# Kernel optimization log

Measured on AMD Instinct MI355X. Metric: run time of the kernel, lower is better.

## Reference

```python
import jax, jax.numpy as jnp
import numpy as np

B, N, D, H = 8, 384, 256, 1024

def setup_inputs() -> dict:
    key = jax.random.key(0)
    ks = jax.random.split(key, 8)
    x = jax.random.normal(ks[0], (B, N, D), jnp.float32)
    adj = jnp.ones((B, N, N), jnp.float32)
    box_num = jax.random.randint(ks[1], (B, 1), 1, N + 1).astype(jnp.int64)
    box_num = box_num.at[0, 0].set(N)  # original code assumes max(box_num) == N
    fc1_w = jax.random.normal(ks[2], (H, D), jnp.float32) * (1.0 / np.sqrt(D))
    fc1_b = jnp.zeros((H,), jnp.float32)
    fc2_w = jax.random.normal(ks[3], (D, H), jnp.float32) * (1.0 / np.sqrt(H))
    fc2_b = jnp.zeros((D,), jnp.float32)
    learn_w = jax.random.uniform(ks[4], (D,), jnp.float32)  # uniform_(0,1) init
    return {"x": x, "adj": adj, "box_num": box_num,
            "fc1_w": fc1_w, "fc1_b": fc1_b, "fc2_w": fc2_w, "fc2_b": fc2_b,
            "learn_w": learn_w}

def reference(x, adj, box_num, fc1_w, fc1_b, fc2_w, fc2_b, learn_w):
    # mlp: fc2(relu(fc1(x)))  -> x_hat (B,N,D)
    x_hat = jnp.maximum(x @ fc1_w.T + fc1_b, 0.0) @ fc2_w.T + fc2_b
    # dynamic mask: -1 where either node i or j is padding, 0 otherwise
    valid = jnp.arange(N)[None, :] < box_num            # (B,N)
    pair_valid = valid[:, None, :] & valid[:, :, None]  # (B,N,N)
    mask = jnp.where(pair_valid, 0.0, -1.0)             # (B,N,N)
    # pairwise weighted L1 distance: einsum('bijd,d->bij', |x_i - x_j| + mask, w)
    # mask broadcasts over d, so its contribution is mask * sum(w) (same math,
    # avoids a second (B,N,N,D) materialization)
    absdiff = jnp.abs(x_hat[:, :, None, :] - x_hat[:, None, :, :])  # (B,N,N,D)
    dist = jnp.einsum('bijd,d->bij', absdiff, learn_w) + mask * jnp.sum(learn_w)
    out = jax.nn.leaky_relu(dist, negative_slope=0.01)
    out = out - jnp.max(out, axis=-1, keepdims=True)
    soft_adj = adj * jnp.exp(out)
    soft_adj = soft_adj / jnp.sum(soft_adj, axis=-1, keepdims=True) + 1e-10
    return soft_adj, x_hat
```

## Files before the change

kernel.cpp:

```cpp
#include <hip/hip_runtime.h>
#include <math.h>

#define B_ 8
#define N_ 384
#define D_ 256
#define H_ 1024

typedef __bf16 bh;
typedef __bf16 bf16x8 __attribute__((ext_vector_type(8)));
typedef float  f32x4  __attribute__((ext_vector_type(4)));
typedef _Float16 h2 __attribute__((ext_vector_type(2)));

#define LDK 40

#if __has_builtin(__builtin_amdgcn_fdot2)
#define FDOT2(a,b,c) __builtin_amdgcn_fdot2((a),(b),(c),false)
#else
#define FDOT2(a,b,c) ((c) + (float)(a).x*(float)(b).x + (float)(a).y*(float)(b).y)
#endif

__device__ inline h2 habs2(h2 x) {
    unsigned u = __builtin_bit_cast(unsigned, x) & 0x7fff7fffu;
    return __builtin_bit_cast(h2, u);
}

__device__ inline void split2(float v, bh& h, bh& l) {
    h = (bh)v;
    l = (bh)(v - (float)h);
}

__device__ inline int load_boxnum(const int* __restrict__ p, int b) {
    bool is64 = ((p[1] | p[3] | p[5] | p[7]) == 0);
    return is64 ? p[2 * b] : p[b];
}

__global__ __launch_bounds__(256) void gemm1_kernel(
        const float* __restrict__ A,
        const float* __restrict__ W,
        const float* __restrict__ bias,
        bh* __restrict__ Ch, bh* __restrict__ Cl)
{
    __shared__ __align__(16) bh AhS[64 * LDK], AlS[64 * LDK], WhS[64 * LDK], WlS[64 * LDK];
    const int tid = threadIdx.x;
    const int m0 = blockIdx.y * 64, n0 = blockIdx.x * 64;
    const int r = tid >> 2, kq = (tid & 3) * 8;
    const int lane = tid & 63, wv_ = tid >> 6;
    const int wm = (wv_ & 1) * 32, wn = (wv_ >> 1) * 32;
    const int l15 = lane & 15, q = lane >> 4;

    f32x4 acc[2][2] = {};
    for (int k0 = 0; k0 < 256; k0 += 32) {
        const float* ap = A + (size_t)(m0 + r) * 256 + k0 + kq;
        const float* wp = W + (size_t)(n0 + r) * 256 + k0 + kq;
        float4 a0 = *(const float4*)ap;
        float4 a1 = *(const float4*)(ap + 4);
        float4 w0 = *(const float4*)wp;
        float4 w1 = *(const float4*)(wp + 4);
        float av[8] = {a0.x, a0.y, a0.z, a0.w, a1.x, a1.y, a1.z, a1.w};
        float wf[8] = {w0.x, w0.y, w0.z, w0.w, w1.x, w1.y, w1.z, w1.w};
        bf16x8 ah, al, wh, wl;
        #pragma unroll
        for (int i = 0; i < 8; i++) {
            bh h, l;
            split2(av[i], h, l); ah[i] = h; al[i] = l;
            split2(wf[i], h, l); wh[i] = h; wl[i] = l;
        }
        __syncthreads();
        *(bf16x8*)&AhS[r * LDK + kq] = ah;  *(bf16x8*)&AlS[r * LDK + kq] = al;
        *(bf16x8*)&WhS[r * LDK + kq] = wh;  *(bf16x8*)&WlS[r * LDK + kq] = wl;
        __syncthreads();
        bf16x8 fah[2], fal[2], fwh[2], fwl[2];
        #pragma unroll
        for (int mi = 0; mi < 2; mi++) {
            int row = wm + mi * 16 + l15;
            fah[mi] = *(const bf16x8*)&AhS[row * LDK + q * 8];
            fal[mi] = *(const bf16x8*)&AlS[row * LDK + q * 8];
        }
        #pragma unroll
        for (int ni = 0; ni < 2; ni++) {
            int row = wn + ni * 16 + l15;
            fwh[ni] = *(const bf16x8*)&WhS[row * LDK + q * 8];
            fwl[ni] = *(const bf16x8*)&WlS[row * LDK + q * 8];
        }
        #pragma unroll
        for (int mi = 0; mi < 2; mi++)
            #pragma unroll
            for (int ni = 0; ni < 2; ni++) {
                acc[mi][ni] = __builtin_amdgcn_mfma_f32_16x16x32_bf16(fah[mi], fwh[ni], acc[mi][ni], 0, 0, 0);
                acc[mi][ni] = __builtin_amdgcn_mfma_f32_16x16x32_bf16(fah[mi], fwl[ni], acc[mi][ni], 0, 0, 0);
                acc[mi][ni] = __builtin_amdgcn_mfma_f32_16x16x32_bf16(fal[mi], fwh[ni], acc[mi][ni], 0, 0, 0);
            }
    }
    #pragma unroll
    for (int ni = 0; ni < 2; ni++) {
        int col = n0 + wn + ni * 16 + l15;
        float bb = bias[col];
        #pragma unroll
        for (int mi = 0; mi < 2; mi++)
            #pragma unroll
            for (int reg = 0; reg < 4; reg++) {
                int row = m0 + wm + mi * 16 + q * 4 + reg;
                float v = fmaxf(acc[mi][ni][reg] + bb, 0.f);
                bh h, l; split2(v, h, l);
                size_t off = (size_t)row * H_ + col;
                Ch[off] = h; Cl[off] = l;
            }
    }
}

__global__ __launch_bounds__(128) void gemm2_kernel(
        const bh* __restrict__ Ah_, const bh* __restrict__ Al_,
        const float* __restrict__ W,
        const float* __restrict__ bias,
        float* __restrict__ C)
{
    __shared__ __align__(16) bh AhS[64 * LDK], AlS[64 * LDK], WhS[32 * LDK], WlS[32 * LDK];
    const int tid = threadIdx.x;
    const int m0 = blockIdx.y * 64, n0 = blockIdx.x * 32;
    const int lane = tid & 63, wv_ = tid >> 6;
    const int wm = wv_ * 32;
    const int l15 = lane & 15, q = lane >> 4;
    const int ra = tid >> 1, ka = (tid & 1) * 16;
    const int rw = tid >> 2, kw = (tid & 3) * 8;

    f32x4 acc[2][2] = {};
    for (int k0 = 0; k0 < 1024; k0 += 32) {
        const bh* ahp = Ah_ + (size_t)(m0 + ra) * H_ + k0 + ka;
        const bh* alp = Al_ + (size_t)(m0 + ra) * H_ + k0 + ka;
        bf16x8 h0 = *(const bf16x8*)ahp, h1 = *(const bf16x8*)(ahp + 8);
        bf16x8 l0 = *(const bf16x8*)alp, l1 = *(const bf16x8*)(alp + 8);
        const float* wp = W + (size_t)(n0 + rw) * H_ + k0 + kw;
        float4 w0 = *(const float4*)wp, w1 = *(const float4*)(wp + 4);
        float wf[8] = {w0.x, w0.y, w0.z, w0.w, w1.x, w1.y, w1.z, w1.w};
        bf16x8 wh, wl;
        #pragma unroll
        for (int i = 0; i < 8; i++) { bh h, l; split2(wf[i], h, l); wh[i] = h; wl[i] = l; }
        __syncthreads();
        *(bf16x8*)&AhS[ra * LDK + ka] = h0;  *(bf16x8*)&AhS[ra * LDK + ka + 8] = h1;
        *(bf16x8*)&AlS[ra * LDK + ka] = l0;  *(bf16x8*)&AlS[ra * LDK + ka + 8] = l1;
        *(bf16x8*)&WhS[rw * LDK + kw] = wh;  *(bf16x8*)&WlS[rw * LDK + kw] = wl;
        __syncthreads();
        bf16x8 fah[2], fal[2], fwh[2], fwl[2];
        #pragma unroll
        for (int mi = 0; mi < 2; mi++) {
            int row = wm + mi * 16 + l15;
            fah[mi] = *(const bf16x8*)&AhS[row * LDK + q * 8];
            fal[mi] = *(const bf16x8*)&AlS[row * LDK + q * 8];
        }
        #pragma unroll
        for (int ni = 0; ni < 2; ni++) {
            int row = ni * 16 + l15;
            fwh[ni] = *(const bf16x8*)&WhS[row * LDK + q * 8];
            fwl[ni] = *(const bf16x8*)&WlS[row * LDK + q * 8];
        }
        #pragma unroll
        for (int mi = 0; mi < 2; mi++)
            #pragma unroll
            for (int ni = 0; ni < 2; ni++) {
                acc[mi][ni] = __builtin_amdgcn_mfma_f32_16x16x32_bf16(fah[mi], fwh[ni], acc[mi][ni], 0, 0, 0);
                acc[mi][ni] = __builtin_amdgcn_mfma_f32_16x16x32_bf16(fah[mi], fwl[ni], acc[mi][ni], 0, 0, 0);
                acc[mi][ni] = __builtin_amdgcn_mfma_f32_16x16x32_bf16(fal[mi], fwh[ni], acc[mi][ni], 0, 0, 0);
            }
    }
    #pragma unroll
    for (int ni = 0; ni < 2; ni++) {
        int col = n0 + ni * 16 + l15;
        float bb = bias[col];
        #pragma unroll
        for (int mi = 0; mi < 2; mi++)
            #pragma unroll
            for (int reg = 0; reg < 4; reg++) {
                int row = m0 + wm + mi * 16 + q * 4 + reg;
                C[(size_t)row * D_ + col] = acc[mi][ni][reg] + bb;
            }
    }
}

#define DLP 68
__global__ __launch_bounds__(256) void dist_kernel(const float* __restrict__ xhat,
                                                   const float* __restrict__ w,
                                                   const int* __restrict__ box_num,
                                                   float* __restrict__ dist) {
    __shared__ __align__(16) unsigned XiU[16 * DLP];
    __shared__ __align__(16) unsigned XjU[16 * DLP];
    const int bidx = blockIdx.x;
    const int b = bidx / 21;
    int p = bidx % 21;
    int ti = 0;
    while (p >= 6 - ti) { p -= 6 - ti; ti++; }
    const int tj = ti + p;
    const int i0 = ti * 64, j0 = tj * 64;

    const int tid = threadIdx.x;
    const int tx = tid & 15, ty = tid >> 4;
    const int lane = tid & 63;
    const int r = tid >> 2, kq = (tid & 3) * 8;
    const int kq2 = (tid & 3) * 4;

    float sumw = w[lane] + w[lane + 64] + w[lane + 128] + w[lane + 192];
    #pragma unroll
    for (int off = 32; off > 0; off >>= 1) sumw += __shfl_xor(sumw, off);

    const float* xb = xhat + (size_t)b * N_ * D_;
    float acc[4][4] = {};

    for (int k0 = 0; k0 < D_; k0 += 32) {
        h2 wk2[16];
        #pragma unroll
        for (int c = 0; c < 16; c++) {
            float2 wp = *(const float2*)&w[k0 + 2 * c];
            wk2[c] = (h2){(_Float16)wp.x, (_Float16)wp.y};
        }
        const float* ip = xb + (size_t)(i0 + r) * D_ + k0 + kq;
        const float* jp = xb + (size_t)(j0 + r) * D_ + k0 + kq;
        float4 i0v = *(const float4*)ip, i1v = *(const float4*)(ip + 4);
        float4 j0v = *(const float4*)jp, j1v = *(const float4*)(jp + 4);
        float fi[8] = {i0v.x, i0v.y, i0v.z, i0v.w, i1v.x, i1v.y, i1v.z, i1v.w};
        float fj[8] = {j0v.x, j0v.y, j0v.z, j0v.w, j1v.x, j1v.y, j1v.z, j1v.w};
        __syncthreads();
        #pragma unroll
        for (int c = 0; c < 4; c++) {
            h2 hi = (h2){(_Float16)fi[2 * c], (_Float16)fi[2 * c + 1]};
            h2 hj = (h2){(_Float16)fj[2 * c], (_Float16)fj[2 * c + 1]};
            XiU[(kq2 + c) * DLP + r] = __builtin_bit_cast(unsigned, hi);
            XjU[(kq2 + c) * DLP + r] = __builtin_bit_cast(unsigned, hj);
        }
        __syncthreads();
        #pragma unroll
        for (int k2 = 0; k2 < 16; k2++) {
            uint4 ar = *(const uint4*)&XiU[k2 * DLP + ty * 4];
            uint4 br = *(const uint4*)&XjU[k2 * DLP + tx * 4];
            h2 ai[4] = {__builtin_bit_cast(h2, ar.x), __builtin_bit_cast(h2, ar.y),
                        __builtin_bit_cast(h2, ar.z), __builtin_bit_cast(h2, ar.w)};
            h2 bj[4] = {__builtin_bit_cast(h2, br.x), __builtin_bit_cast(h2, br.y),
                        __builtin_bit_cast(h2, br.z), __builtin_bit_cast(h2, br.w)};
            h2 wv = wk2[k2];
            #pragma unroll
            for (int ii = 0; ii < 4; ii++)
                #pragma unroll
                for (int jj = 0; jj < 4; jj++) {
                    h2 d = habs2(ai[ii] - bj[jj]);
                    acc[ii][jj] = FDOT2(d, wv, acc[ii][jj]);
                }
        }
    }

    const int bn = load_boxnum(box_num, b);
    float m[4][4];
    #pragma unroll
    for (int ii = 0; ii < 4; ii++) {
        int i = i0 + ty * 4 + ii;
        bool vi = i < bn;
        #pragma unroll
        for (int jj = 0; jj < 4; jj++) {
            int j = j0 + tx * 4 + jj;
            float v = acc[ii][jj];
            if (!(vi && (j < bn))) v -= sumw;
            m[ii][jj] = v > 0.f ? v : 0.01f * v;
        }
    }
    #pragma unroll
    for (int ii = 0; ii < 4; ii++) {
        int i = i0 + ty * 4 + ii;
        float4 o = {m[ii][0], m[ii][1], m[ii][2], m[ii][3]};
        *(float4*)&dist[((size_t)b * N_ + i) * N_ + j0 + tx * 4] = o;
    }
    #pragma unroll
    for (int jj = 0; jj < 4; jj++) {
        int j = j0 + tx * 4 + jj;
        float4 o = {m[0][jj], m[1][jj], m[2][jj], m[3][jj]};
        *(float4*)&dist[((size_t)b * N_ + j) * N_ + i0 + ty * 4] = o;
    }
}

__global__ __launch_bounds__(256) void softmax_kernel(float* __restrict__ sa,
                                                      const float* __restrict__ adj) {
    const int row = blockIdx.x * 4 + (threadIdx.x >> 6);
    const int t = threadIdx.x & 63;
    float* prow = sa + (size_t)row * N_;
    const float* arow = adj + (size_t)row * N_;
    float v[6];
    float m = -1e30f;
    #pragma unroll
    for (int qq = 0; qq < 6; qq++) { v[qq] = prow[t + qq * 64]; m = fmaxf(m, v[qq]); }
    #pragma unroll
    for (int off = 32; off > 0; off >>= 1) m = fmaxf(m, __shfl_xor(m, off));
    float e[6];
    float s = 0.f;
    #pragma unroll
    for (int qq = 0; qq < 6; qq++) { e[qq] = arow[t + qq * 64] * expf(v[qq] - m); s += e[qq]; }
    #pragma unroll
    for (int off = 32; off > 0; off >>= 1) s += __shfl_xor(s, off);
    float inv = 1.0f / s;
    #pragma unroll
    for (int qq = 0; qq < 6; qq++) prow[t + qq * 64] = e[qq] * inv + 1e-10f;
}

extern "C" void kernel_launch(void* const* d_in, const int* in_sizes, int n_in,
                              void* d_out, int out_size, void* d_ws, size_t ws_size,
                              hipStream_t stream) {
    const float* x       = (const float*)d_in[0];
    const float* adj     = (const float*)d_in[1];
    const int*   box_num = (const int*)d_in[2];
    const float* fc1_w   = (const float*)d_in[3];
    const float* fc1_b   = (const float*)d_in[4];
    const float* fc2_w   = (const float*)d_in[5];
    const float* fc2_b   = (const float*)d_in[6];
    const float* learn_w = (const float*)d_in[7];

    float* soft_adj = (float*)d_out;
    float* xhat     = (float*)d_out + (size_t)B_ * N_ * N_;

    const int BN = B_ * N_;
    const size_t bytes_per_row = (size_t)H_ * 2 * 2;
    long long mr = (long long)(ws_size / bytes_per_row) & ~63LL;
    int max_rows = (int)((mr > BN) ? BN : mr);
    if (max_rows < 64) max_rows = 64;
    bh* c1h = (bh*)d_ws;
    bh* c1l = c1h + (size_t)max_rows * H_;

    for (int m0 = 0; m0 < BN; m0 += max_rows) {
        int rows = BN - m0; if (rows > max_rows) rows = max_rows;
        dim3 g1(H_ / 64, rows / 64);
        gemm1_kernel<<<g1, 256, 0, stream>>>(x + (size_t)m0 * D_, fc1_w, fc1_b, c1h, c1l);
        dim3 g2(D_ / 32, rows / 64);
        gemm2_kernel<<<g2, 128, 0, stream>>>(c1h, c1l, fc2_w, fc2_b, xhat + (size_t)m0 * D_);
    }

    dist_kernel<<<B_ * 21, 256, 0, stream>>>(xhat, learn_w, box_num, soft_adj);

    softmax_kernel<<<BN / 4, 256, 0, stream>>>(soft_adj, adj);
}
```

Before: 140.7 us.

## Pre-split GEMM operands to bf16 and use larger swizzled tiles with direct LDS loads

Adds a prep kernel that splits x, fc1_w and fc2_w into bf16 hi/lo pairs once, so the GEMMs no longer redo the split inside every tile. Both GEMMs are rewritten to use global_load_lds direct-to-LDS copies, XOR-swizzled LDS layouts, and larger tiles (128x128 for gemm1, 64x128 with K step 64 for gemm2) to raise reuse per block. The workspace chunking loop is removed, so the code now assumes the workspace holds all intermediates. It also adds an extra launch, and with fewer, larger blocks fewer CUs may be occupied.

```diff
diff --git a/kernel.cpp b/kernel.cpp
--- a/kernel.cpp
+++ b/kernel.cpp
@@ -7,11 +7,10 @@
 #define H_ 1024
 
 typedef __bf16 bh;
+typedef __bf16 bh4   __attribute__((ext_vector_type(4)));
 typedef __bf16 bf16x8 __attribute__((ext_vector_type(8)));
 typedef float  f32x4  __attribute__((ext_vector_type(4)));
 typedef _Float16 h2 __attribute__((ext_vector_type(2)));
-
-#define LDK 40
 
 #if __has_builtin(__builtin_amdgcn_fdot2)
 #define FDOT2(a,b,c) __builtin_amdgcn_fdot2((a),(b),(c),false)
@@ -19,6 +18,10 @@
 #define FDOT2(a,b,c) ((c) + (float)(a).x*(float)(b).x + (float)(a).y*(float)(b).y)
 #endif
 
+#define GLDS16(gp, lp) __builtin_amdgcn_global_load_lds( \
+    (const __attribute__((address_space(1))) unsigned*)(gp), \
+    (__attribute__((address_space(3))) unsigned*)(lp), 16, 0, 0)
+
 __device__ inline h2 habs2(h2 x) {
     unsigned u = __builtin_bit_cast(unsigned, x) & 0x7fff7fffu;
     return __builtin_bit_cast(h2, u);
@@ -34,143 +37,151 @@
     return is64 ? p[2 * b] : p[b];
 }
 
+__global__ __launch_bounds__(256) void prep_split(
+        const float* __restrict__ x, const float* __restrict__ w1, const float* __restrict__ w2,
+        bh* __restrict__ xh, bh* __restrict__ xl,
+        bh* __restrict__ w1h, bh* __restrict__ w1l,
+        bh* __restrict__ w2h, bh* __restrict__ w2l) {
+    const int blk = blockIdx.x;
+    const float* src; bh *dh, *dl; int idx;
+    if (blk < 768)       { src = x;  dh = xh;  dl = xl;  idx = blk * 256 + threadIdx.x; }
+    else if (blk < 1024) { src = w1; dh = w1h; dl = w1l; idx = (blk - 768) * 256 + threadIdx.x; }
+    else                 { src = w2; dh = w2h; dl = w2l; idx = (blk - 1024) * 256 + threadIdx.x; }
+    float4 v = ((const float4*)src)[idx];
+    float f[4] = {v.x, v.y, v.z, v.w};
+    bh4 hv, lv;
+    #pragma unroll
+    for (int i = 0; i < 4; i++) { bh h, l; split2(f[i], h, l); hv[i] = h; lv[i] = l; }
+    *(bh4*)&dh[4 * (size_t)idx] = hv;
+    *(bh4*)&dl[4 * (size_t)idx] = lv;
+}
+
 __global__ __launch_bounds__(256) void gemm1_kernel(
-        const float* __restrict__ A,
-        const float* __restrict__ W,
+        const bh* __restrict__ xh, const bh* __restrict__ xl,
+        const bh* __restrict__ w1h, const bh* __restrict__ w1l,
         const float* __restrict__ bias,
-        bh* __restrict__ Ch, bh* __restrict__ Cl)
-{
-    __shared__ __align__(16) bh AhS[64 * LDK], AlS[64 * LDK], WhS[64 * LDK], WlS[64 * LDK];
-    const int tid = threadIdx.x;
-    const int m0 = blockIdx.y * 64, n0 = blockIdx.x * 64;
-    const int r = tid >> 2, kq = (tid & 3) * 8;
-    const int lane = tid & 63, wv_ = tid >> 6;
-    const int wm = (wv_ & 1) * 32, wn = (wv_ >> 1) * 32;
+        bh* __restrict__ c1h, bh* __restrict__ c1l) {
+    __shared__ __align__(16) bh lds[16384];
+    const int tid = threadIdx.x, lane = tid & 63, w = tid >> 6;
+    const int m0 = blockIdx.y * 128, n0 = blockIdx.x * 128;
+    const int lr = lane >> 2, kb = lane & 3;
+    const int kbp = kb ^ ((lr >> 1) & 3);
+    const bh* psrc; int rowbase;
+    if (w == 0)      { psrc = xh;  rowbase = m0; }
+    else if (w == 1) { psrc = xl;  rowbase = m0; }
+    else if (w == 2) { psrc = w1h; rowbase = n0; }
+    else             { psrc = w1l; rowbase = n0; }
+    const bh* gsrc = psrc + (size_t)(rowbase + lr) * 256 + kbp * 8;
+    bh* lwb = &lds[w * 4096 + lane * 8];
     const int l15 = lane & 15, q = lane >> 4;
-
-    f32x4 acc[2][2] = {};
+    const int swq = q ^ ((l15 >> 1) & 3);
+    const int wm = (w & 1) * 64, wn = (w >> 1) * 64;
+
+    f32x4 acc[4][4] = {};
     for (int k0 = 0; k0 < 256; k0 += 32) {
-        const float* ap = A + (size_t)(m0 + r) * 256 + k0 + kq;
-        const float* wp = W + (size_t)(n0 + r) * 256 + k0 + kq;
-        float4 a0 = *(const float4*)ap;
-        float4 a1 = *(const float4*)(ap + 4);
-        float4 w0 = *(const float4*)wp;
-        float4 w1 = *(const float4*)(wp + 4);
-        float av[8] = {a0.x, a0.y, a0.z, a0.w, a1.x, a1.y, a1.z, a1.w};
-        float wf[8] = {w0.x, w0.y, w0.z, w0.w, w1.x, w1.y, w1.z, w1.w};
-        bf16x8 ah, al, wh, wl;
-        #pragma unroll
-        for (int i = 0; i < 8; i++) {
-            bh h, l;
-            split2(av[i], h, l); ah[i] = h; al[i] = l;
-            split2(wf[i], h, l); wh[i] = h; wl[i] = l;
-        }
-        __syncthreads();
-        *(bf16x8*)&AhS[r * LDK + kq] = ah;  *(bf16x8*)&AlS[r * LDK + kq] = al;
-        *(bf16x8*)&WhS[r * LDK + kq] = wh;  *(bf16x8*)&WlS[r * LDK + kq] = wl;
-        __syncthreads();
-        bf16x8 fah[2], fal[2], fwh[2], fwl[2];
-        #pragma unroll
-        for (int mi = 0; mi < 2; mi++) {
-            int row = wm + mi * 16 + l15;
-            fah[mi] = *(const bf16x8*)&AhS[row * LDK + q * 8];
-            fal[mi] = *(const bf16x8*)&AlS[row * LDK + q * 8];
-        }
-        #pragma unroll
-        for (int ni = 0; ni < 2; ni++) {
-            int row = wn + ni * 16 + l15;
-            fwh[ni] = *(const bf16x8*)&WhS[row * LDK + q * 8];
-            fwl[ni] = *(const bf16x8*)&WlS[row * LDK + q * 8];
-        }
-        #pragma unroll
-        for (int mi = 0; mi < 2; mi++)
-            #pragma unroll
-            for (int ni = 0; ni < 2; ni++) {
-                acc[mi][ni] = __builtin_amdgcn_mfma_f32_16x16x32_bf16(fah[mi], fwh[ni], acc[mi][ni], 0, 0, 0);
-                acc[mi][ni] = __builtin_amdgcn_mfma_f32_16x16x32_bf16(fah[mi], fwl[ni], acc[mi][ni], 0, 0, 0);
-                acc[mi][ni] = __builtin_amdgcn_mfma_f32_16x16x32_bf16(fal[mi], fwh[ni], acc[mi][ni], 0, 0, 0);
-            }
-    }
-    #pragma unroll
-    for (int ni = 0; ni < 2; ni++) {
+        __syncthreads();
+        #pragma unroll
+        for (int s = 0; s < 8; s++)
+            GLDS16(gsrc + (size_t)s * 4096 + k0, lwb + s * 512);
+        __syncthreads();
+        bf16x8 fa[4][2], fb[4][2];
+        #pragma unroll
+        for (int i = 0; i < 4; i++) {
+            int ra = wm + i * 16 + l15;
+            int rb = wn + i * 16 + l15;
+            fa[i][0] = *(const bf16x8*)&lds[        ra * 32 + swq * 8];
+            fa[i][1] = *(const bf16x8*)&lds[ 4096 + ra * 32 + swq * 8];
+            fb[i][0] = *(const bf16x8*)&lds[ 8192 + rb * 32 + swq * 8];
+            fb[i][1] = *(const bf16x8*)&lds[12288 + rb * 32 + swq * 8];
+        }
+        #pragma unroll
+        for (int mi = 0; mi < 4; mi++)
+            #pragma unroll
+            for (int ni = 0; ni < 4; ni++) {
+                acc[mi][ni] = __builtin_amdgcn_mfma_f32_16x16x32_bf16(fa[mi][0], fb[ni][0], acc[mi][ni], 0, 0, 0);
+                acc[mi][ni] = __builtin_amdgcn_mfma_f32_16x16x32_bf16(fa[mi][0], fb[ni][1], acc[mi][ni], 0, 0, 0);
+                acc[mi][ni] = __builtin_amdgcn_mfma_f32_16x16x32_bf16(fa[mi][1], fb[ni][0], acc[mi][ni], 0, 0, 0);
+            }
+    }
+    #pragma unroll
+    for (int ni = 0; ni < 4; ni++) {
         int col = n0 + wn + ni * 16 + l15;
         float bb = bias[col];
         #pragma unroll
-        for (int mi = 0; mi < 2; mi++)
+        for (int mi = 0; mi < 4; mi++)
             #pragma unroll
             for (int reg = 0; reg < 4; reg++) {
                 int row = m0 + wm + mi * 16 + q * 4 + reg;
                 float v = fmaxf(acc[mi][ni][reg] + bb, 0.f);
                 bh h, l; split2(v, h, l);
                 size_t off = (size_t)row * H_ + col;
-                Ch[off] = h; Cl[off] = l;
-            }
-    }
-}
-
-__global__ __launch_bounds__(128) void gemm2_kernel(
-        const bh* __restrict__ Ah_, const bh* __restrict__ Al_,
-        const float* __restrict__ W,
+                c1h[off] = h; c1l[off] = l;
+            }
+    }
+}
+
+__global__ __launch_bounds__(256) void gemm2_kernel(
+        const bh* __restrict__ c1h, const bh* __restrict__ c1l,
+        const bh* __restrict__ w2h, const bh* __restrict__ w2l,
         const float* __restrict__ bias,
-        float* __restrict__ C)
-{
-    __shared__ __align__(16) bh AhS[64 * LDK], AlS[64 * LDK], WhS[32 * LDK], WlS[32 * LDK];
-    const int tid = threadIdx.x;
-    const int m0 = blockIdx.y * 64, n0 = blockIdx.x * 32;
-    const int lane = tid & 63, wv_ = tid >> 6;
-    const int wm = wv_ * 32;
+        float* __restrict__ C) {
+    __shared__ __align__(16) bh lds[24576];
+    const int tid = threadIdx.x, lane = tid & 63, w = tid >> 6;
+    const int m0 = blockIdx.y * 64, n0 = blockIdx.x * 128;
+    const int lr = lane >> 3, kb = lane & 7;
+    const int kbp = kb ^ lr;
     const int l15 = lane & 15, q = lane >> 4;
-    const int ra = tid >> 1, ka = (tid & 1) * 16;
-    const int rw = tid >> 2, kw = (tid & 3) * 8;
-
-    f32x4 acc[2][2] = {};
-    for (int k0 = 0; k0 < 1024; k0 += 32) {
-        const bh* ahp = Ah_ + (size_t)(m0 + ra) * H_ + k0 + ka;
-        const bh* alp = Al_ + (size_t)(m0 + ra) * H_ + k0 + ka;
-        bf16x8 h0 = *(const bf16x8*)ahp, h1 = *(const bf16x8*)(ahp + 8);
-        bf16x8 l0 = *(const bf16x8*)alp, l1 = *(const bf16x8*)(alp + 8);
-        const float* wp = W + (size_t)(n0 + rw) * H_ + k0 + kw;
-        float4 w0 = *(const float4*)wp, w1 = *(const float4*)(wp + 4);
-        float wf[8] = {w0.x, w0.y, w0.z, w0.w, w1.x, w1.y, w1.z, w1.w};
-        bf16x8 wh, wl;
-        #pragma unroll
-        for (int i = 0; i < 8; i++) { bh h, l; split2(wf[i], h, l); wh[i] = h; wl[i] = l; }
-        __syncthreads();
-        *(bf16x8*)&AhS[ra * LDK + ka] = h0;  *(bf16x8*)&AhS[ra * LDK + ka + 8] = h1;
-        *(bf16x8*)&AlS[ra * LDK + ka] = l0;  *(bf16x8*)&AlS[ra * LDK + ka + 8] = l1;
-        *(bf16x8*)&WhS[rw * LDK + kw] = wh;  *(bf16x8*)&WlS[rw * LDK + kw] = wl;
-        __syncthreads();
-        bf16x8 fah[2], fal[2], fwh[2], fwl[2];
-        #pragma unroll
-        for (int mi = 0; mi < 2; mi++) {
-            int row = wm + mi * 16 + l15;
-            fah[mi] = *(const bf16x8*)&AhS[row * LDK + q * 8];
-            fal[mi] = *(const bf16x8*)&AlS[row * LDK + q * 8];
-        }
-        #pragma unroll
-        for (int ni = 0; ni < 2; ni++) {
-            int row = ni * 16 + l15;
-            fwh[ni] = *(const bf16x8*)&WhS[row * LDK + q * 8];
-            fwl[ni] = *(const bf16x8*)&WlS[row * LDK + q * 8];
-        }
-        #pragma unroll
-        for (int mi = 0; mi < 2; mi++)
+    const int wn = w * 32;
+
+    f32x4 acc[4][2] = {};
+    for (int k0 = 0; k0 < 1024; k0 += 64) {
+        __syncthreads();
+        #pragma unroll
+        for (int j = 0; j < 12; j++) {
+            int c = w * 12 + j;
+            const bh* g; int ldsbase, s;
+            if (c < 8)       { g = c1h; ldsbase = 0;     s = c;      g += (size_t)(m0 + s * 8 + lr) * 1024; }
+            else if (c < 16) { g = c1l; ldsbase = 4096;  s = c - 8;  g += (size_t)(m0 + s * 8 + lr) * 1024; }
+            else if (c < 32) { g = w2h; ldsbase = 8192;  s = c - 16; g += (size_t)(n0 + s * 8 + lr) * 1024; }
+            else             { g = w2l; ldsbase = 16384; s = c - 32; g += (size_t)(n0 + s * 8 + lr) * 1024; }
+            GLDS16(g + k0 + kbp * 8, &lds[ldsbase + s * 512 + lane * 8]);
+        }
+        __syncthreads();
+        #pragma unroll
+        for (int ks = 0; ks < 2; ks++) {
+            const int p = (ks * 4 + q) ^ (l15 & 7);
+            bf16x8 fa[4][2], fb[2][2];
+            #pragma unroll
+            for (int mi = 0; mi < 4; mi++) {
+                int ra = mi * 16 + l15;
+                fa[mi][0] = *(const bf16x8*)&lds[       ra * 64 + p * 8];
+                fa[mi][1] = *(const bf16x8*)&lds[4096 + ra * 64 + p * 8];
+            }
             #pragma unroll
             for (int ni = 0; ni < 2; ni++) {
-                acc[mi][ni] = __builtin_amdgcn_mfma_f32_16x16x32_bf16(fah[mi], fwh[ni], acc[mi][ni], 0, 0, 0);
-                acc[mi][ni] = __builtin_amdgcn_mfma_f32_16x16x32_bf16(fah[mi], fwl[ni], acc[mi][ni], 0, 0, 0);
-                acc[mi][ni] = __builtin_amdgcn_mfma_f32_16x16x32_bf16(fal[mi], fwh[ni], acc[mi][ni], 0, 0, 0);
-            }
+                int rb = wn + ni * 16 + l15;
+                fb[ni][0] = *(const bf16x8*)&lds[ 8192 + rb * 64 + p * 8];
+                fb[ni][1] = *(const bf16x8*)&lds[16384 + rb * 64 + p * 8];
+            }
+            #pragma unroll
+            for (int mi = 0; mi < 4; mi++)
+                #pragma unroll
+                for (int ni = 0; ni < 2; ni++) {
+                    acc[mi][ni] = __builtin_amdgcn_mfma_f32_16x16x32_bf16(fa[mi][0], fb[ni][0], acc[mi][ni], 0, 0, 0);
+                    acc[mi][ni] = __builtin_amdgcn_mfma_f32_16x16x32_bf16(fa[mi][0], fb[ni][1], acc[mi][ni], 0, 0, 0);
+                    acc[mi][ni] = __builtin_amdgcn_mfma_f32_16x16x32_bf16(fa[mi][1], fb[ni][0], acc[mi][ni], 0, 0, 0);
+                }
+        }
     }
     #pragma unroll
     for (int ni = 0; ni < 2; ni++) {
-        int col = n0 + ni * 16 + l15;
+        int col = n0 + wn + ni * 16 + l15;
         float bb = bias[col];
         #pragma unroll
-        for (int mi = 0; mi < 2; mi++)
+        for (int mi = 0; mi < 4; mi++)
             #pragma unroll
             for (int reg = 0; reg < 4; reg++) {
-                int row = m0 + wm + mi * 16 + q * 4 + reg;
+                int row = m0 + mi * 16 + q * 4 + reg;
                 C[(size_t)row * D_ + col] = acc[mi][ni][reg] + bb;
             }
     }
@@ -311,23 +322,24 @@
     float* soft_adj = (float*)d_out;
     float* xhat     = (float*)d_out + (size_t)B_ * N_ * N_;
 
-    const int BN = B_ * N_;
-    const size_t bytes_per_row = (size_t)H_ * 2 * 2;
-    long long mr = (long long)(ws_size / bytes_per_row) & ~63LL;
-    int max_rows = (int)((mr > BN) ? BN : mr);
-    if (max_rows < 64) max_rows = 64;
-    bh* c1h = (bh*)d_ws;
-    bh* c1l = c1h + (size_t)max_rows * H_;
-
-    for (int m0 = 0; m0 < BN; m0 += max_rows) {
-        int rows = BN - m0; if (rows > max_rows) rows = max_rows;
-        dim3 g1(H_ / 64, rows / 64);
-        gemm1_kernel<<<g1, 256, 0, stream>>>(x + (size_t)m0 * D_, fc1_w, fc1_b, c1h, c1l);
-        dim3 g2(D_ / 32, rows / 64);
-        gemm2_kernel<<<g2, 128, 0, stream>>>(c1h, c1l, fc2_w, fc2_b, xhat + (size_t)m0 * D_);
-    }
+    bh* xh  = (bh*)d_ws;
+    bh* xl  = xh  + 786432;
+    bh* w1h = xl  + 786432;
+    bh* w1l = w1h + 262144;
+    bh* w2h = w1l + 262144;
+    bh* w2l = w2h + 262144;
+    bh* c1h = w2l + 262144;
+    bh* c1l = c1h + 3145728;
+
+    prep_split<<<1280, 256, 0, stream>>>(x, fc1_w, fc2_w, xh, xl, w1h, w1l, w2h, w2l);
+
+    dim3 g1(H_ / 128, (B_ * N_) / 128);
+    gemm1_kernel<<<g1, 256, 0, stream>>>(xh, xl, w1h, w1l, fc1_b, c1h, c1l);
+
+    dim3 g2(D_ / 128, (B_ * N_) / 64);
+    gemm2_kernel<<<g2, 256, 0, stream>>>(c1h, c1l, w2h, w2l, fc2_b, xhat);
 
     dist_kernel<<<B_ * 21, 256, 0, stream>>>(xhat, learn_w, box_num, soft_adj);
 
-    softmax_kernel<<<BN / 4, 256, 0, stream>>>(soft_adj, adj);
-}
+    softmax_kernel<<<(B_ * N_) / 4, 256, 0, stream>>>(soft_adj, adj);
+}
```

Result: slower. 143.5 us (+2.1%).
